# Kernel optimization log

Measured on AMD Instinct MI355X. Metric: run time of the kernel, lower is better.

## Reference

```python
import jax, jax.numpy as jnp
import numpy as np

E = 512   # embed_size == hidden_size (required: step-0 'embed' is the init output of size hidden)
H = 512
A = 512   # attention dim
V = 20000
P = 196
B = 128
T = 24


def setup_inputs() -> dict:
    key = jax.random.key(0)
    ks = jax.random.split(key, 20)
    s = 0.02
    return {
        "features": jax.random.normal(ks[0], (B, P, E), jnp.float32),
        "captions": jax.random.randint(ks[1], (B, T), 0, V),
        "emb": jax.random.normal(ks[2], (V, E), jnp.float32) * s,
        "W_init_h": jax.random.normal(ks[3], (E, H), jnp.float32) * s,
        "b_init_h": jnp.zeros((H,), jnp.float32),
        "W_init_o": jax.random.normal(ks[4], (E, H), jnp.float32) * s,
        "b_init_o": jnp.zeros((H,), jnp.float32),
        "Wf": jax.random.normal(ks[5], (E, A), jnp.float32) * s,
        "bf": jnp.zeros((A,), jnp.float32),
        "Wh": jax.random.normal(ks[6], (H, A), jnp.float32) * s,
        "bh": jnp.zeros((A,), jnp.float32),
        "v_att": jax.random.normal(ks[7], (A,), jnp.float32) * s,
        "W_ih": jax.random.normal(ks[8], (3 * H, 2 * E), jnp.float32) * s,
        "W_hh": jax.random.normal(ks[9], (3 * H, H), jnp.float32) * s,
        "b_ih": jnp.zeros((3 * H,), jnp.float32),
        "b_hh": jnp.zeros((3 * H,), jnp.float32),
        "W_out": jax.random.normal(ks[10], (V, H), jnp.float32) * s,
        "b_out": jnp.zeros((V,), jnp.float32),
    }


def reference(features, emb, W_init_h, b_init_h, W_init_o, b_init_o,
              Wf, bf, Wh, bh, v_att, W_ih, W_hh, b_ih, b_hh,
              W_out, b_out, captions):
    # init_hidden_state
    avg = features.mean(axis=1)                          # [B,E]
    hidden0 = jnp.tanh(avg @ W_init_h + b_init_h)        # [B,H]
    output0 = jnp.tanh(avg @ W_init_o + b_init_o)        # [B,H]

    emb_caps = emb[captions]                             # [B,T,E]
    # teacher forcing: step 0 uses init output, step i>0 uses embeddings[:, i-1]
    embed_seq = jnp.concatenate([output0[:, None, :], emb_caps[:, :-1, :]], axis=1)
    xs = embed_seq.transpose(1, 0, 2)                    # [T,B,E]

    feat_proj = features @ Wf + bf                       # [B,P,A] (precompute attn key proj)

    def step(h, x_emb):
        # additive attention over pixels
        score = jnp.tanh(feat_proj + (h @ Wh + bh)[:, None, :]) @ v_att   # [B,P]
        alpha = jax.nn.softmax(score, axis=1)
        ctx = jnp.einsum('bp,bpe->be', alpha, features)                   # [B,E]
        x = jnp.concatenate([x_emb, ctx], axis=1)                         # [B,2E]
        # single-step GRU (PyTorch gate order r,z,n)
        gi = x @ W_ih.T + b_ih
        gh = h @ W_hh.T + b_hh
        gi_r, gi_z, gi_n = jnp.split(gi, 3, axis=1)
        gh_r, gh_z, gh_n = jnp.split(gh, 3, axis=1)
        r = jax.nn.sigmoid(gi_r + gh_r)
        z = jax.nn.sigmoid(gi_z + gh_z)
        n = jnp.tanh(gi_n + r * gh_n)
        h_new = (1.0 - z) * n + z * h
        pred = h_new @ W_out.T + b_out                                    # [B,V]
        return h_new, pred

    _, preds = jax.lax.scan(step, hidden0, xs)           # preds: [T,B,V]
    return preds.transpose(1, 0, 2)                      # [B,T,V]
```

## Files before the change

### kernel.cpp

```cpp
#include <hip/hip_runtime.h>

#define Bb 128
#define Tt 24
#define Ee 512
#define Hh 512
#define Aa 512
#define Vv 20000
#define Pp 196
#define TV (Tt*Vv)
#define NBLK 512
#define NTHR 256
#define GT (NBLK*NTHR)
#define SMEM_BYTES 65536

typedef __attribute__((ext_vector_type(8))) short bfrag;
typedef __attribute__((ext_vector_type(4))) float f4;
typedef __attribute__((ext_vector_type(4))) unsigned short us4;

#define MFMA16(a,b,c) __builtin_amdgcn_mfma_f32_16x16x32_bf16(a,b,c,0,0,0)

__device__ __forceinline__ unsigned short f2bf(float f){
  unsigned int x = __builtin_bit_cast(unsigned int, f);
  x += 0x7fffu + ((x >> 16) & 1u);
  return (unsigned short)(x >> 16);
}
__device__ __forceinline__ float bfu2f(unsigned short u){
  unsigned int x = ((unsigned int)u) << 16;
  return __builtin_bit_cast(float, x);
}
#define LOG2E 1.442695041f
__device__ __forceinline__ float fexp2(float x){ return __builtin_amdgcn_exp2f(x); }
__device__ __forceinline__ float frcp (float x){ return __builtin_amdgcn_rcpf(x); }
__device__ __forceinline__ float tanh_f(float x){ return 1.0f - 2.0f*frcp(1.0f + fexp2((2.0f*LOG2E)*x)); }
__device__ __forceinline__ float sigm_f(float x){ return frcp(1.0f + fexp2(-LOG2E*x)); }

__device__ __forceinline__ unsigned long long scld8(const void* p){
  return __hip_atomic_load((const unsigned long long*)p, __ATOMIC_RELAXED, __HIP_MEMORY_SCOPE_AGENT);
}
__device__ __forceinline__ unsigned scld4(const unsigned* p){
  return __hip_atomic_load(p, __ATOMIC_RELAXED, __HIP_MEMORY_SCOPE_AGENT);
}
__device__ __forceinline__ void scst4(unsigned* p, unsigned v){
  __hip_atomic_store(p, v, __ATOMIC_RELAXED, __HIP_MEMORY_SCOPE_AGENT);
}
__device__ __forceinline__ void scstf(float* p, float v){
  __hip_atomic_store(p, v, __ATOMIC_RELAXED, __HIP_MEMORY_SCOPE_AGENT);
}

__device__ __forceinline__ void set_flag(unsigned* line, unsigned v){
  asm volatile("s_waitcnt vmcnt(0)" ::: "memory");
  __syncthreads();
  if(threadIdx.x == 0) scst4(line, v);
}
__device__ __forceinline__ void poll_flags(const unsigned* base, int n, unsigned tgt){
  int tid = threadIdx.x;
  for(;;){
    int ok = (tid < n) ? (scld4(base + tid*16) >= tgt) : 1;
    if(__syncthreads_count(ok) == NTHR) break;
    __builtin_amdgcn_s_sleep(2);
  }
  asm volatile("" ::: "memory");
}

__device__ __forceinline__ void gbar2(unsigned* sync, unsigned phase){
  __syncthreads();
  int tid = threadIdx.x, blk = blockIdx.x;
  if(tid == 0)
    (void)__hip_atomic_fetch_add(sync + (blk & 31)*16, 1u,
                                 __ATOMIC_RELEASE, __HIP_MEMORY_SCOPE_AGENT);
  if(blk == 0){
    for(;;){
      int ok = (tid < 32) ? (scld4(sync + tid*16) >= phase*16u) : 1;
      if(__syncthreads_count(ok) == NTHR) break;
      __builtin_amdgcn_s_sleep(2);
    }
    if(tid == 0) scst4(sync + 32*16, phase);
  }
  if(tid == 0){
    while(scld4(sync + 32*16) < phase) __builtin_amdgcn_s_sleep(2);
    (void)__hip_atomic_load(sync + 32*16, __ATOMIC_ACQUIRE, __HIP_MEMORY_SCOPE_AGENT);
  }
  __syncthreads();
}

__global__ void k_zero(unsigned* s){
  int i = blockIdx.x*256 + threadIdx.x;
  s[i] = 0u;
}

__device__ __forceinline__ void cast_loop(const float* __restrict__ s,
                                          unsigned short* __restrict__ d,
                                          int n4, int gtid){
  for(int i = gtid; i < n4; i += GT){
    float4 v = ((const float4*)s)[i];
    us4 o; o[0]=f2bf(v.x); o[1]=f2bf(v.y); o[2]=f2bf(v.z); o[3]=f2bf(v.w);
    ((us4*)d)[i] = o;
  }
}
__device__ __forceinline__ void tr_tile(const float* __restrict__ S,
                                        unsigned short* __restrict__ D,
                                        int it, int jt, int tid, float (*T)[33]){
  int er = tid>>3, c4 = (tid&7)*4;
  float4 v = *(const float4*)(S + (size_t)(jt*32+er)*512 + it*32 + c4);
  T[er][c4+0]=v.x; T[er][c4+1]=v.y; T[er][c4+2]=v.z; T[er][c4+3]=v.w;
  __syncthreads();
  us4 o;
  o[0]=f2bf(T[c4+0][er]); o[1]=f2bf(T[c4+1][er]);
  o[2]=f2bf(T[c4+2][er]); o[3]=f2bf(T[c4+3][er]);
  *(us4*)(D + (size_t)(it*32+er)*512 + jt*32 + c4) = o;
  __syncthreads();
}

__device__ __forceinline__ void stage16(char* dstSM, const unsigned short* src, int R0){
  int tid = threadIdx.x;
  #pragma unroll
  for(int j=0;j<8;j++){
    int u = tid + j*256;
    int row = u >> 7, c8 = u & 127;
    unsigned long long q = scld8(src + (size_t)(R0+row)*Hh + c8*4);
    int bo = (row<<10) + (c8<<3);
    bo ^= (row&7)<<4;
    *(unsigned long long*)(dstSM + bo) = q;
  }
}


__device__ void attention_task(int b, const float* __restrict__ hpr_t,
                               const unsigned short* __restrict__ fpb,
                               const unsigned short* __restrict__ featsB,
                               const float* __restrict__ vatt,
                               unsigned short* __restrict__ ctx_t, char* SM)
{
  float* hp  = (float*)SM;
  float* vp  = hp + 512;
  float* sc  = vp + 512;
  float* red = sc + 200;
  int tid = threadIdx.x;
  {
    unsigned long long q = scld8(hpr_t + (size_t)b*Aa + tid*2);
    float2 hv = __builtin_bit_cast(float2, q);
    float2 vv = *(const float2*)(vatt + tid*2);
    int a0 = tid*2, a1 = a0+1;
    hp[((a0&31)<<4)+(a0>>5)] = hv.x;
    hp[((a1&31)<<4)+(a1>>5)] = hv.y;
    vp[((a0&31)<<4)+(a0>>5)] = vv.x;
    vp[((a1&31)<<4)+(a1>>5)] = vv.y;
  }
  __syncthreads();
  int grp = tid >> 4, gl = tid & 15;
  for(int pass=0; pass<13; pass++){
    int p = pass*16 + grp;
    float acc = 0.0f;
    if(p < Pp){
      const unsigned short* fr = fpb + ((size_t)b*Pp + p)*Aa + gl*32;
      #pragma unroll
      for(int j=0;j<32;j+=8){
        bfrag fv = *(const bfrag*)(fr + j);
        #pragma unroll
        for(int q=0;q<8;q++){
          int idx = ((j+q)<<4) + gl;
          float x = bfu2f((unsigned short)fv[q]) + hp[idx];
          acc += tanh_f(x) * vp[idx];
        }
      }
    }
    acc += __shfl_xor(acc, 1, 64);
    acc += __shfl_xor(acc, 2, 64);
    acc += __shfl_xor(acc, 4, 64);
    acc += __shfl_xor(acc, 8, 64);
    if(p < Pp && gl == 0) sc[p] = acc;
  }
  __syncthreads();
  if(tid < 64){
    float m = -1e30f;
    for(int i=0;i<4;i++){ int p = tid + i*64; if(p < Pp) m = fmaxf(m, sc[p]); }
    for(int off=1; off<64; off<<=1) m = fmaxf(m, __shfl_xor(m, off, 64));
    float s = 0.0f;
    for(int i=0;i<4;i++){ int p = tid + i*64; if(p < Pp) s += fexp2((sc[p]-m)*LOG2E); }
    for(int off=1; off<64; off<<=1) s += __shfl_xor(s, off, 64);
    if(tid == 0){ red[0] = m; red[1] = frcp(s); }
  }
  __syncthreads();
  float mx = red[0], rS = red[1];
  float al_t = 0.0f;
  if(tid < Pp) al_t = fexp2((sc[tid]-mx)*LOG2E) * rS;
  __syncthreads();
  if(tid < Pp) sc[tid] = al_t;
  __syncthreads();
  float c0 = 0.f, c1 = 0.f;
  const unsigned int* fb = (const unsigned int*)(featsB + (size_t)b*Pp*Ee);
  #pragma unroll 4
  for(int p=0;p<Pp;p++){
    float al = sc[p];
    unsigned int u = fb[(size_t)p*256 + tid];
    unsigned int lo = (u & 0xffffu) << 16, hi = u & 0xffff0000u;
    c0 += al * __builtin_bit_cast(float, lo);
    c1 += al * __builtin_bit_cast(float, hi);
  }
  unsigned int cw = ((unsigned int)f2bf(c1) << 16) | (unsigned int)f2bf(c0);
  scst4((unsigned*)ctx_t + (size_t)b*256 + tid, cw);
}

__device__ void hproj_mfma(int R0, int HC0, const char* SMh,
                           const unsigned short* __restrict__ WhT,
                           const float* __restrict__ bhv, float* __restrict__ hpr)
{
  int tid = threadIdx.x;
  int w = tid>>6, l = tid&63, l16 = l&15, lk = l>>4;
  int a = HC0 + w*16 + l16;
  f4 acc = (f4)(0.0f);
  for(int k0=0;k0<512;k0+=32){
    int koff = k0 + lk*8;
    int bo = (l16<<10) + (koff<<1); bo ^= (l16&7)<<4;
    bfrag ah = *(const bfrag*)(SMh + bo);
    bfrag bq = *(const bfrag*)(WhT + (size_t)a*Hh + koff);
    acc = MFMA16(ah, bq, acc);
  }
  float bias = bhv[a];
  #pragma unroll
  for(int i=0;i<4;i++){
    int row = lk*4 + i;
    scstf(hpr + (size_t)(R0+row)*Aa + a, acc[i] + bias);
  }
}

__device__ void gates_phaseA(int R0, int HC0, const unsigned short* __restrict__ eseqT,
                             const unsigned short* __restrict__ WihB,
                             const unsigned short* __restrict__ WhhB,
                             const char* SMh, f4 (&agh)[3], f4 (&agi)[3])
{
  int tid = threadIdx.x;
  int w = tid>>6, l = tid&63, l16 = l&15, lk = l>>4;
  int hcol = HC0 + w*16 + l16;
  #pragma unroll
  for(int q=0;q<3;q++){ agh[q]=(f4)(0.f); agi[q]=(f4)(0.f); }
  for(int k0=0;k0<512;k0+=32){
    int koff = k0 + lk*8;
    int bo = (l16<<10) + (koff<<1); bo ^= (l16&7)<<4;
    bfrag ah = *(const bfrag*)(SMh + bo);
    bfrag ae = *(const bfrag*)(eseqT + (size_t)(R0+l16)*Ee + koff);
    #pragma unroll
    for(int q=0;q<3;q++){
      int jj = q*512 + hcol;
      bfrag bh_ = *(const bfrag*)(WhhB + (size_t)jj*512  + koff);
      bfrag be  = *(const bfrag*)(WihB + (size_t)jj*1024 + koff);
      agh[q] = MFMA16(ah, bh_, agh[q]);
      agi[q] = MFMA16(ae, be,  agi[q]);
    }
  }
}

__device__ void gates_phaseB(int R0, int HC0, const char* SMc,
                             const unsigned short* __restrict__ WihB,
                             const float* __restrict__ bih, const float* __restrict__ bhh,
                             const float* __restrict__ hf_cur, float* __restrict__ hf_nxt,
                             unsigned short* __restrict__ hbU_nxt,
                             f4 (&agh)[3], f4 (&agi)[3], unsigned short* HBp)
{
  int tid = threadIdx.x;
  int w = tid>>6, l = tid&63, l16 = l&15, lk = l>>4;
  int hcol = HC0 + w*16 + l16;
  for(int k0=0;k0<512;k0+=32){
    int koff = k0 + lk*8;
    int bo = (l16<<10) + (koff<<1); bo ^= (l16&7)<<4;
    bfrag ac = *(const bfrag*)(SMc + bo);
    #pragma unroll
    for(int q=0;q<3;q++){
      int jj = q*512 + hcol;
      bfrag bc = *(const bfrag*)(WihB + (size_t)jj*1024 + 512 + koff);
      agi[q] = MFMA16(ac, bc, agi[q]);
    }
  }
  float bir = bih[hcol],      bhr = bhh[hcol];
  float biz = bih[512+hcol],  bhz = bhh[512+hcol];
  float bin = bih[1024+hcol], bhn = bhh[1024+hcol];
  #pragma unroll
  for(int i=0;i<4;i++){
    int row = lk*4 + i;
    int b = R0 + row;
    float r_ = sigm_f(agi[0][i] + bir + agh[0][i] + bhr);
    float z_ = sigm_f(agi[1][i] + biz + agh[1][i] + bhz);
    float n_ = tanh_f(agi[2][i] + bin + r_*(agh[2][i] + bhn));
    float ho = hf_cur[(size_t)b*Hh + hcol];
    float hn = (1.0f - z_)*n_ + z_*ho;
    hf_nxt[(size_t)b*Hh + hcol] = hn;
    HBp[row*88 + w*16 + l16] = f2bf(hn);
  }
  __syncthreads();
  #pragma unroll
  for(int j=0;j<2;j++){
    int widx = tid + j*256;
    int row = widx >> 5, pr = widx & 31;
    unsigned uu = (unsigned)HBp[row*88 + pr*2] | ((unsigned)HBp[row*88 + pr*2+1] << 16);
    scst4((unsigned*)(hbU_nxt + (size_t)(R0+row)*Hh + HC0) + pr, uu);
  }
}

__device__ void pred_pair(int pt, int twA,
                          const unsigned short* __restrict__ hbA,
                          const unsigned short* __restrict__ hbB,
                          const unsigned short* __restrict__ WoutB,
                          const float* __restrict__ bout, float* __restrict__ out,
                          char* SM)
{
  int tid = threadIdx.x;
  int vchunk = pt >> 2, mbase = (pt & 3)*32;
  #pragma unroll
  for(int j=0;j<16;j++){
    int u = tid + j*256;
    int row = u >> 7, c8 = u & 127;
    unsigned long long qa = scld8(hbA + (size_t)(mbase+row)*Hh + c8*4);
    unsigned long long qb = scld8(hbB + (size_t)(mbase+row)*Hh + c8*4);
    int bo = (row<<10) + (c8<<3);
    bo ^= (row&7)<<4;
    *(unsigned long long*)(SM + bo) = qa;
    *(unsigned long long*)(SM + 32768 + bo) = qb;
  }
  __syncthreads();
  int w = tid>>6, l = tid&63, l16 = l&15, lk = l>>4;
  int nb = vchunk*256 + w*64;
  f4 accA[2][4], accB[2][4];
  #pragma unroll
  for(int mi=0;mi<2;mi++) for(int ni=0;ni<4;ni++){ accA[mi][ni]=(f4)(0.0f); accB[mi][ni]=(f4)(0.0f); }
  for(int k0=0;k0<512;k0+=32){
    int koff = k0 + lk*8;
    bfrag afA[2], afB[2], bq[4];
    #pragma unroll
    for(int mi=0;mi<2;mi++){
      int row = mi*16 + l16;
      int bo = (row<<10) + (koff<<1);
      bo ^= (row&7)<<4;
      afA[mi] = *(const bfrag*)(SM + bo);
      afB[mi] = *(const bfrag*)(SM + 32768 + bo);
    }
    #pragma unroll
    for(int ni=0;ni<4;ni++){
      int v = nb + ni*16 + l16; if(v > Vv-1) v = Vv-1;
      bq[ni] = *(const bfrag*)(WoutB + (size_t)v*Hh + koff);
    }
    #pragma unroll
    for(int mi=0;mi<2;mi++)
      #pragma unroll
      for(int ni=0;ni<4;ni++){
        accA[mi][ni] = MFMA16(afA[mi], bq[ni], accA[mi][ni]);
        accB[mi][ni] = MFMA16(afB[mi], bq[ni], accB[mi][ni]);
      }
  }
  #pragma unroll
  for(int ni=0;ni<4;ni++){
    int v = nb + ni*16 + l16;
    if(v < Vv){
      float bias = bout[v];
      #pragma unroll
      for(int mi=0;mi<2;mi++){
        #pragma unroll
        for(int i=0;i<4;i++){
          int br = mbase + mi*16 + lk*4 + i;
          __builtin_nontemporal_store(accA[mi][ni][i] + bias,
              out + (size_t)br*TV + (size_t)twA*Vv + v);
          __builtin_nontemporal_store(accB[mi][ni][i] + bias,
              out + (size_t)br*TV + (size_t)(twA+1)*Vv + v);
        }
      }
    }
  }
  __syncthreads();
}

__global__ __launch_bounds__(NTHR, 2) void k_all(
    const float* feats, const int* caps, const float* emb,
    const float* Winh, const float* binh, const float* Wino, const float* bino,
    const float* Wf, const float* bfv, const float* Wh, const float* bhv,
    const float* vatt, const float* Wih, const float* Whh,
    const float* bih, const float* bhh, const float* Wout, const float* bout,
    float* out,
    float* hfR, unsigned short* hbU, float* hpr,
    unsigned short* ctxR, unsigned short* avgB, unsigned short* eseq,
    unsigned short* WfT, unsigned short* WhT,
    unsigned short* WinhT, unsigned short* WinoT,
    unsigned short* WihB, unsigned short* WhhB,
    unsigned short* fpb, unsigned short* featsB, unsigned short* WoutB,
    unsigned* sync)
{
  extern __shared__ char SMEM[];
  const int blk = blockIdx.x, tid = threadIdx.x;
  const int gtid = blk*NTHR + tid;
  unsigned* flagsA = sync + 40*16;
  unsigned* flagsG = sync + 168*16;
  unsigned* flagsP = sync + 240*16;
  unsigned* aggP   = sync + 304*16;
  float* h_f0 = hfR;
  unsigned short* h_b0 = hbU;

  cast_loop(Wih,  WihB,  (3*Hh*2*Ee)/4, gtid);
  cast_loop(Whh,  WhhB,  (3*Hh*Hh)/4,   gtid);
  cast_loop(Wout, WoutB, (Vv*Hh)/4,     gtid);
  cast_loop(feats,featsB,(Bb*Pp*Ee)/4,  gtid);
  for(int task = blk; task < 1024; task += NBLK){
    int z = task >> 8, rt = task & 255;
    int it = rt & 15, jt = rt >> 4;
    const float* S = (z==0)?Wf:(z==1)?Wh:(z==2)?Winh:Wino;
    unsigned short* D = (z==0)?WfT:(z==1)?WhT:(z==2)?WinhT:WinoT;
    tr_tile(S, D, it, jt, tid, (float(*)[33])SMEM);
  }
  if(blk < Bb){
    int b = blk;
    const float* fb = feats + (size_t)b*Pp*Ee;
    float a0=0.f, a1=0.f;
    for(int p=0;p<Pp;p++){
      float2 v = *(const float2*)(fb + (size_t)p*Ee + tid*2);
      a0 += v.x; a1 += v.y;
    }
    a0 *= (1.0f/Pp); a1 *= (1.0f/Pp);
    unsigned int pack = ((unsigned int)f2bf(a1)<<16) | (unsigned int)f2bf(a0);
    ((unsigned int*)avgB)[(size_t)b*256 + tid] = pack;
  }
  for(int task = blk; task < (Tt-1)*Bb; task += NBLK){
    int ts = task/Bb + 1, b = task%Bb;
    int cap = caps[b*Tt + (ts-1)];
    float2 v = *(const float2*)(emb + (size_t)cap*Ee + tid*2);
    unsigned int pack = ((unsigned int)f2bf(v.y)<<16) | (unsigned int)f2bf(v.x);
    ((unsigned int*)(eseq + ((size_t)ts*Bb + b)*Ee))[tid] = pack;
  }
  gbar2(sync, 1);

  for(int task = blk; task < 1584; task += NBLK){
    int w = tid>>6, l = tid&63, l16 = l&15, lk = l>>4;
    if(task < 1568){
      int bx = task % 196, by = task / 196;
      size_t m_base = (size_t)bx*128 + (w&1)*64;
      int nb = by*64 + (w>>1)*32;
      f4 acc[4][2];
      #pragma unroll
      for(int mi=0;mi<4;mi++) for(int ni=0;ni<2;ni++) acc[mi][ni] = (f4)(0.0f);
      for(int k0=0;k0<512;k0+=32){
        int koff = k0 + lk*8;
        bfrag af[4], bq[2];
        #pragma unroll
        for(int mi=0;mi<4;mi++) af[mi] = *(const bfrag*)(featsB + (m_base+mi*16+l16)*512 + koff);
        #pragma unroll
        for(int ni=0;ni<2;ni++) bq[ni] = *(const bfrag*)(WfT + (size_t)(nb+ni*16+l16)*512 + koff);
        #pragma unroll
        for(int mi=0;mi<4;mi++)
          #pragma unroll
          for(int ni=0;ni<2;ni++)
            acc[mi][ni] = MFMA16(af[mi], bq[ni], acc[mi][ni]);
      }
      #pragma unroll
      for(int ni=0;ni<2;ni++){
        int a = nb + ni*16 + l16;
        float bias = bfv[a];
        #pragma unroll
        for(int mi=0;mi<4;mi++){
          size_t r = m_base + mi*16 + lk*4;
          #pragma unroll
          for(int i=0;i<4;i++)
            fpb[(r+i)*512 + a] = f2bf(acc[mi][ni][i] + bias);
        }
      }
    } else {
      int idx = task - 1568;
      int y = idx >> 3, xb = idx & 7;
      int m0 = (w&1)*64, nb = xb*64 + (w>>1)*32;
      const unsigned short* Wt = y ? WinoT : WinhT;
      const float* bias = y ? bino : binh;
      f4 acc[4][2];
      #pragma unroll
      for(int mi=0;mi<4;mi++) for(int ni=0;ni<2;ni++) acc[mi][ni] = (f4)(0.0f);
      for(int k0=0;k0<512;k0+=32){
        int koff = k0 + lk*8;
        bfrag af[4], bq[2];
        #pragma unroll
        for(int mi=0;mi<4;mi++) af[mi] = *(const bfrag*)(avgB + (size_t)(m0+mi*16+l16)*512 + koff);
        #pragma unroll
        for(int ni=0;ni<2;ni++) bq[ni] = *(const bfrag*)(Wt + (size_t)(nb+ni*16+l16)*512 + koff);
        #pragma unroll
        for(int mi=0;mi<4;mi++)
          #pragma unroll
          for(int ni=0;ni<2;ni++)
            acc[mi][ni] = MFMA16(af[mi], bq[ni], acc[mi][ni]);
      }
      #pragma unroll
      for(int ni=0;ni<2;ni++){
        int n = nb + ni*16 + l16;
        float bv = bias[n];
        #pragma unroll
        for(int mi=0;mi<4;mi++){
          int bb = m0 + mi*16 + lk*4;
          #pragma unroll
          for(int i=0;i<4;i++){
            float val = tanh_f(acc[mi][ni][i] + bv);
            if(y==0){ h_f0[(size_t)(bb+i)*Hh + n] = val; h_b0[(size_t)(bb+i)*Hh + n] = f2bf(val); }
            else    { eseq[(size_t)(bb+i)*Ee + n] = f2bf(val); }
          }
        }
      }
    }
  }
  gbar2(sync, 2);

  int xcd = blk & 7, slot = blk >> 3;

  if(slot < 16){
    int b = slot*8 + xcd;
    int rg = b >> 4;
    for(int t=0; t<Tt; t++){
      poll_flags(flagsP + rg*8*16, 8, (unsigned)(t+1));
      attention_task(b, hpr + (size_t)(t&1)*Bb*Aa, fpb, featsB, vatt,
                     ctxR + (size_t)(t&3)*Bb*Ee, SMEM);
      set_flag(flagsA + b*16, (unsigned)(t+1));
    }
  } else if(slot < 24){
    int r = slot - 16, c = xcd;
    int R0 = r*16, HC0 = c*64;
    char* SMh = SMEM;
    char* SMc = SMEM + 16384;
    unsigned short* HBp = (unsigned short*)(SMEM + 32768);
    f4 agh[3], agi[3];
    stage16(SMh, hbU, R0);
    __syncthreads();
    hproj_mfma(R0, HC0, SMh, WhT, bhv, hpr);
    set_flag(flagsP + (r*8+c)*16, 1u);
    gates_phaseA(R0, HC0, eseq, WihB, WhhB, SMh, agh, agi);
    for(int t=0; t<Tt; t++){
      poll_flags(flagsA + R0*16, 16, (unsigned)(t+1));
      stage16(SMc, ctxR + (size_t)(t&3)*Bb*Ee, R0);
      __syncthreads();
      gates_phaseB(R0, HC0, SMc, WihB, bih, bhh,
                   hfR + (size_t)(t&1)*Bb*Hh, hfR + (size_t)((t+1)&1)*Bb*Hh,
                   hbU + (size_t)(t+1)*Bb*Hh, agh, agi, HBp);
      set_flag(flagsG + (r*8+c)*16, (unsigned)(t+1));
      if(t+1 < Tt){
        poll_flags(flagsG + r*8*16, 8, (unsigned)(t+1));
        stage16(SMh, hbU + (size_t)(t+1)*Bb*Hh, R0);
        __syncthreads();
        hproj_mfma(R0, HC0, SMh, WhT, bhv, hpr + (size_t)((t+1)&1)*Bb*Aa);
        set_flag(flagsP + (r*8+c)*16, (unsigned)(t+2));
        gates_phaseA(R0, HC0, eseq + (size_t)(t+1)*Bb*Ee, WihB, WhhB, SMh, agh, agi);
      }
    }
  } else {
    int ps = slot - 24;
    int pt = xcd*40 + ps;
    if(ps == 0){
      for(int pp=0; pp<12; pp++){
        int t1 = 2*pp + 2;
        poll_flags(flagsG, 64, (unsigned)t1);
        if(tid == 0) scst4(aggP + xcd*16, (unsigned)t1);
        pred_pair(pt, 2*pp, hbU + (size_t)(2*pp+1)*Bb*Hh,
                  hbU + (size_t)(2*pp+2)*Bb*Hh, WoutB, bout, out, SMEM);
      }
    } else if(pt < 316){
      for(int pp=0; pp<12; pp++){
        int t1 = 2*pp + 2;
        poll_flags(aggP + xcd*16, 1, (unsigned)t1);
        pred_pair(pt, 2*pp, hbU + (size_t)(2*pp+1)*Bb*Hh,
                  hbU + (size_t)(2*pp+2)*Bb*Hh, WoutB, bout, out, SMEM);
      }
    }
  }
}

extern "C" void kernel_launch(void* const* d_in, const int* in_sizes, int n_in,
                              void* d_out, int out_size, void* d_ws, size_t ws_size,
                              hipStream_t stream)
{
  const float* feats = (const float*)d_in[0];
  const int*   caps  = (const int*)d_in[1];
  const float* emb   = (const float*)d_in[2];
  const float* Winh  = (const float*)d_in[3];
  const float* binh  = (const float*)d_in[4];
  const float* Wino  = (const float*)d_in[5];
  const float* bino  = (const float*)d_in[6];
  const float* Wf    = (const float*)d_in[7];
  const float* bfv   = (const float*)d_in[8];
  const float* Wh    = (const float*)d_in[9];
  const float* bhv   = (const float*)d_in[10];
  const float* vatt  = (const float*)d_in[11];
  const float* Wih   = (const float*)d_in[12];
  const float* Whh   = (const float*)d_in[13];
  const float* bih   = (const float*)d_in[14];
  const float* bhh   = (const float*)d_in[15];
  const float* Wout  = (const float*)d_in[16];
  const float* bout  = (const float*)d_in[17];
  float* out = (float*)d_out;

  char* ws = (char*)d_ws;
  size_t off = 0;
  auto alloc = [&](size_t bytes){
    off = (off + 255) & ~(size_t)255;
    void* p = ws + off; off += bytes; return p;
  };
  unsigned* syncp = (unsigned*)alloc(32768);
  float* hfR = (float*)alloc((size_t)2*Bb*Hh*4);
  unsigned short* hbU = (unsigned short*)alloc((size_t)(Tt+1)*Bb*Hh*2);
  float* hpr = (float*)alloc((size_t)2*Bb*Aa*4);
  unsigned short* ctxR  = (unsigned short*)alloc((size_t)4*Bb*Ee*2);
  unsigned short* avgB  = (unsigned short*)alloc((size_t)Bb*Ee*2);
  unsigned short* eseq  = (unsigned short*)alloc((size_t)Tt*Bb*Ee*2);
  unsigned short* WfT   = (unsigned short*)alloc((size_t)Ee*Aa*2);
  unsigned short* WhT   = (unsigned short*)alloc((size_t)Hh*Aa*2);
  unsigned short* WinhT = (unsigned short*)alloc((size_t)Ee*Hh*2);
  unsigned short* WinoT = (unsigned short*)alloc((size_t)Ee*Hh*2);
  unsigned short* WihB  = (unsigned short*)alloc((size_t)3*Hh*2*Ee*2);
  unsigned short* WhhB  = (unsigned short*)alloc((size_t)3*Hh*Hh*2);
  unsigned short* fpb   = (unsigned short*)alloc((size_t)Bb*Pp*Aa*2);
  unsigned short* featsB= (unsigned short*)alloc((size_t)Bb*Pp*Ee*2);
  unsigned short* WoutB = (unsigned short*)alloc((size_t)Vv*Hh*2);
  if(ws_size < off) return;

  k_zero<<<32, 256, 0, stream>>>(syncp);
  k_all<<<NBLK, NTHR, SMEM_BYTES, stream>>>(
      feats, caps, emb, Winh, binh, Wino, bino, Wf, bfv, Wh, bhv, vatt,
      Wih, Whh, bih, bhh, Wout, bout, out,
      hfR, hbU, hpr, ctxR, avgB, eseq,
      WfT, WhT, WinhT, WinoT, WihB, WhhB, fpb, featsB, WoutB, syncp);
}
```

Before: 1.448 ms.

## Fuse h-projection into attention blocks to remove a cross-block sync stage

The attention query projection (h @ Wh) moves out of the GRU-gate blocks and into each attention block, which now computes it redundantly for its own batch row from the staged 16-row hidden tile. This removes the flagsP handoff and the global hpr buffer, so each step's critical path loses one inter-block flag round-trip. In exchange, every attention block does a full 16x512x512 MFMA projection but keeps only one row of it, about sixteen times the needed work, and it rereads all of WhT every step.

New measurement: 1.889 ms. 30.4% more time.

```diff
diff --git a/kernel.cpp b/kernel.cpp
--- a/kernel.cpp
+++ b/kernel.cpp
@@ -43,9 +43,6 @@
 __device__ __forceinline__ void scst4(unsigned* p, unsigned v){
   __hip_atomic_store(p, v, __ATOMIC_RELAXED, __HIP_MEMORY_SCOPE_AGENT);
 }
-__device__ __forceinline__ void scstf(float* p, float v){
-  __hip_atomic_store(p, v, __ATOMIC_RELAXED, __HIP_MEMORY_SCOPE_AGENT);
-}
 
 __device__ __forceinline__ void set_flag(unsigned* line, unsigned v){
   asm volatile("s_waitcnt vmcnt(0)" ::: "memory");
@@ -125,28 +122,38 @@
 }
 
 
-__device__ void attention_task(int b, const float* __restrict__ hpr_t,
-                               const unsigned short* __restrict__ fpb,
+__device__ void hproj_attn(int rw, const char* SMh,
+                           const unsigned short* __restrict__ WhT,
+                           const float* __restrict__ bhv, float* __restrict__ hp)
+{
+  int tid = threadIdx.x;
+  int w = tid>>6, l = tid&63, l16 = l&15, lk = l>>4;
+  int lksel = rw >> 2, isel = rw & 3;
+  #pragma unroll
+  for(int nt8 = 0; nt8 < 8; nt8++){
+    int a = (w*8 + nt8)*16 + l16;
+    f4 acc = (f4)(0.0f);
+    for(int k0=0;k0<512;k0+=32){
+      int koff = k0 + lk*8;
+      int bo = (l16<<10) + (koff<<1); bo ^= (l16&7)<<4;
+      bfrag ah = *(const bfrag*)(SMh + bo);
+      bfrag bq = *(const bfrag*)(WhT + (size_t)a*Hh + koff);
+      acc = MFMA16(ah, bq, acc);
+    }
+    if(lk == lksel){
+      float v = acc[isel] + bhv[a];
+      hp[((a&31)<<4)+(a>>5)] = v;
+    }
+  }
+}
+
+__device__ void attention_core(int b, const unsigned short* __restrict__ fpb,
                                const unsigned short* __restrict__ featsB,
-                               const float* __restrict__ vatt,
-                               unsigned short* __restrict__ ctx_t, char* SM)
+                               unsigned short* __restrict__ ctx_t,
+                               const float* hp, const float* vp,
+                               float* sc, float* red)
 {
-  float* hp  = (float*)SM;
-  float* vp  = hp + 512;
-  float* sc  = vp + 512;
-  float* red = sc + 200;
   int tid = threadIdx.x;
-  {
-    unsigned long long q = scld8(hpr_t + (size_t)b*Aa + tid*2);
-    float2 hv = __builtin_bit_cast(float2, q);
-    float2 vv = *(const float2*)(vatt + tid*2);
-    int a0 = tid*2, a1 = a0+1;
-    hp[((a0&31)<<4)+(a0>>5)] = hv.x;
-    hp[((a1&31)<<4)+(a1>>5)] = hv.y;
-    vp[((a0&31)<<4)+(a0>>5)] = vv.x;
-    vp[((a1&31)<<4)+(a1>>5)] = vv.y;
-  }
-  __syncthreads();
   int grp = tid >> 4, gl = tid & 15;
   for(int pass=0; pass<13; pass++){
     int p = pass*16 + grp;
@@ -199,29 +206,6 @@
   }
   unsigned int cw = ((unsigned int)f2bf(c1) << 16) | (unsigned int)f2bf(c0);
   scst4((unsigned*)ctx_t + (size_t)b*256 + tid, cw);
-}
-
-__device__ void hproj_mfma(int R0, int HC0, const char* SMh,
-                           const unsigned short* __restrict__ WhT,
-                           const float* __restrict__ bhv, float* __restrict__ hpr)
-{
-  int tid = threadIdx.x;
-  int w = tid>>6, l = tid&63, l16 = l&15, lk = l>>4;
-  int a = HC0 + w*16 + l16;
-  f4 acc = (f4)(0.0f);
-  for(int k0=0;k0<512;k0+=32){
-    int koff = k0 + lk*8;
-    int bo = (l16<<10) + (koff<<1); bo ^= (l16&7)<<4;
-    bfrag ah = *(const bfrag*)(SMh + bo);
-    bfrag bq = *(const bfrag*)(WhT + (size_t)a*Hh + koff);
-    acc = MFMA16(ah, bq, acc);
-  }
-  float bias = bhv[a];
-  #pragma unroll
-  for(int i=0;i<4;i++){
-    int row = lk*4 + i;
-    scstf(hpr + (size_t)(R0+row)*Aa + a, acc[i] + bias);
-  }
 }
 
 __device__ void gates_phaseA(int R0, int HC0, const unsigned short* __restrict__ eseqT,
@@ -374,7 +358,7 @@
     const float* vatt, const float* Wih, const float* Whh,
     const float* bih, const float* bhh, const float* Wout, const float* bout,
     float* out,
-    float* hfR, unsigned short* hbU, float* hpr,
+    float* hfR, unsigned short* hbU,
     unsigned short* ctxR, unsigned short* avgB, unsigned short* eseq,
     unsigned short* WfT, unsigned short* WhT,
     unsigned short* WinhT, unsigned short* WinoT,
@@ -387,7 +371,6 @@
   const int gtid = blk*NTHR + tid;
   unsigned* flagsA = sync + 40*16;
   unsigned* flagsG = sync + 168*16;
-  unsigned* flagsP = sync + 240*16;
   unsigned* aggP   = sync + 304*16;
   float* h_f0 = hfR;
   unsigned short* h_b0 = hbU;
@@ -503,11 +486,23 @@
 
   if(slot < 16){
     int b = slot*8 + xcd;
-    int rg = b >> 4;
+    int rg = b >> 4, rw = b & 15;
+    char* SMh = SMEM;
+    float* hp  = (float*)(SMEM + 16384);
+    float* vp  = hp + 512;
+    float* sc  = vp + 512;
+    float* red = sc + 200;
+    { float2 vv = *(const float2*)(vatt + tid*2);
+      int a0 = tid*2, a1 = a0+1;
+      vp[((a0&31)<<4)+(a0>>5)] = vv.x;
+      vp[((a1&31)<<4)+(a1>>5)] = vv.y; }
     for(int t=0; t<Tt; t++){
-      poll_flags(flagsP + rg*8*16, 8, (unsigned)(t+1));
-      attention_task(b, hpr + (size_t)(t&1)*Bb*Aa, fpb, featsB, vatt,
-                     ctxR + (size_t)(t&3)*Bb*Ee, SMEM);
+      if(t > 0) poll_flags(flagsG + rg*8*16, 8, (unsigned)t);
+      stage16(SMh, hbU + (size_t)t*Bb*Hh, rg*16);
+      __syncthreads();
+      hproj_attn(rw, SMh, WhT, bhv, hp);
+      __syncthreads();
+      attention_core(b, fpb, featsB, ctxR + (size_t)(t&3)*Bb*Ee, hp, vp, sc, red);
       set_flag(flagsA + b*16, (unsigned)(t+1));
     }
   } else if(slot < 24){
@@ -519,8 +514,6 @@
     f4 agh[3], agi[3];
     stage16(SMh, hbU, R0);
     __syncthreads();
-    hproj_mfma(R0, HC0, SMh, WhT, bhv, hpr);
-    set_flag(flagsP + (r*8+c)*16, 1u);
     gates_phaseA(R0, HC0, eseq, WihB, WhhB, SMh, agh, agi);
     for(int t=0; t<Tt; t++){
       poll_flags(flagsA + R0*16, 16, (unsigned)(t+1));
@@ -534,8 +527,6 @@
         poll_flags(flagsG + r*8*16, 8, (unsigned)(t+1));
         stage16(SMh, hbU + (size_t)(t+1)*Bb*Hh, R0);
         __syncthreads();
-        hproj_mfma(R0, HC0, SMh, WhT, bhv, hpr + (size_t)((t+1)&1)*Bb*Aa);
-        set_flag(flagsP + (r*8+c)*16, (unsigned)(t+2));
         gates_phaseA(R0, HC0, eseq + (size_t)(t+1)*Bb*Ee, WihB, WhhB, SMh, agh, agi);
       }
     }
@@ -594,7 +585,6 @@
   unsigned* syncp = (unsigned*)alloc(32768);
   float* hfR = (float*)alloc((size_t)2*Bb*Hh*4);
   unsigned short* hbU = (unsigned short*)alloc((size_t)(Tt+1)*Bb*Hh*2);
-  float* hpr = (float*)alloc((size_t)2*Bb*Aa*4);
   unsigned short* ctxR  = (unsigned short*)alloc((size_t)4*Bb*Ee*2);
   unsigned short* avgB  = (unsigned short*)alloc((size_t)Bb*Ee*2);
   unsigned short* eseq  = (unsigned short*)alloc((size_t)Tt*Bb*Ee*2);
@@ -613,6 +603,6 @@
   k_all<<<NBLK, NTHR, SMEM_BYTES, stream>>>(
       feats, caps, emb, Winh, binh, Wino, bino, Wf, bfv, Wh, bhv, vatt,
       Wih, Whh, bih, bhh, Wout, bout, out,
-      hfR, hbU, hpr, ctxR, avgB, eseq,
+      hfR, hbU, ctxR, avgB, eseq,
       WfT, WhT, WinhT, WinoT, WihB, WhhB, fpb, featsB, WoutB, syncp);
 }
```
